# Kernel tuning notes

Measured on AMD Instinct MI355X. Metric: run time of the kernel, lower is better.

## Reference

```python
import jax, jax.numpy as jnp
import numpy as np

W = 10        # hurst window == signature path window (increments)
DELTA_MAX = 1.5
BN_EPS = 1e-5


def _revcumsum(x, axis):
    return jnp.flip(jnp.cumsum(jnp.flip(x, axis), axis=axis), axis)


def _forward(features, hw1, hb1, hw2, hb2, hw3, hb3, gw1, gb1, gw2, gb2,
             p1, p1b, p2, p2b, p3, p3b, p4, p4b,
             w1, b1, gamma, beta, rmean, rvar, w2, b2, w3, b3):
    B, T, d = features.shape
    f32 = features.dtype
    # log returns, left-padded with 0
    lp = features[:, :, 0]
    ret = jnp.pad(lp[:, 1:] - lp[:, :-1], ((0, 0), (1, 0)))
    # Hurst estimator on sliding windows returns[:, t-W:t] for t in [W, T)
    idxh = jnp.arange(T - W)[:, None] + jnp.arange(W)[None, :]
    rw = ret[:, idxh]                                          # [B, T-W, W]
    hh = jax.nn.relu(rw @ hw1 + hb1)
    hh = jax.nn.relu(hh @ hw2 + hb2)
    H_tail = 0.5 * jax.nn.sigmoid((hh @ hw3 + hb3)[..., 0])    # [B, T-W]
    # first W entries copy the t=W estimate (matches torch slice-broadcast)
    H_local = jnp.concatenate([jnp.repeat(H_tail[:, :1], W, axis=1), H_tail], axis=1)
    vol = jnp.cumsum(jnp.abs(ret), axis=1) / (jnp.arange(1, T + 1, dtype=f32) + 1e-8)
    # depth gate from (H_local, vol_local)
    regime = jnp.stack([H_local, vol], axis=-1)                # [B, T, 2]
    gate = jax.nn.softmax(jax.nn.relu(regime @ gw1 + gb1) @ gw2 + gb2, axis=-1)  # [B,T,4]
    # windowed path increments: window at t covers global increments t-W .. t-1
    Dinc = features[:, 1:] - features[:, :-1]                  # [B, T-1, d]
    Dp = jnp.pad(Dinc, ((0, 0), (W, 0), (0, 0)))
    idx = jnp.arange(T)[:, None] + jnp.arange(W)[None, :]
    Dw = Dp[:, idx]                                            # [B, T, W, d] (zero-padded early)
    S = _revcumsum(Dw, 2)                                      # suffix sums S_r = sum_{m>=r} D_m
    lvl1 = S[:, :, 0]                                          # [B, T, d] = path[-1]-path[0]
    # level2 (torch loop) = sum_{i<=m} D_i (x) D_m  (diagonal included)
    A = Dw[..., :, None] * S[..., None, :]                     # [B, T, W, d, d]
    l2f = jnp.sum(A, axis=2).reshape(B, T, d * d)
    # level3 (torch loop) = sum_{i<j<=n} D_i (x) D_j (x) D_n
    RA = _revcumsum(A, 2) - A                                  # exclusive suffix sum of A
    l3f = jnp.einsum('btrd,btref->btdef', Dw, RA).reshape(B, T, d ** 3)
    # level4 = flatten(level2 (x) level2); (d^2)^2 == d^4 so no pad/trunc
    l4f = (l2f[..., :, None] * l2f[..., None, :]).reshape(B, T, d ** 4)
    proj1 = lvl1 @ p1 + p1b
    proj2 = jnp.concatenate([lvl1, l2f], -1) @ p2 + p2b
    proj3 = jnp.concatenate([lvl1, l2f, l3f], -1) @ p3 + p3b
    proj4 = jnp.concatenate([lvl1, l2f, l3f, l4f], -1) @ p4 + p4b
    # depth k active iff path_len >= k+1 i.e. t >= k (k = depth index)
    tv = jnp.arange(T)
    m2 = (tv >= 1).astype(f32)[None, :, None]
    m3 = (tv >= 2).astype(f32)[None, :, None]
    m4 = (tv >= 3).astype(f32)[None, :, None]
    sig_repr = (gate[..., 0:1] * proj1 + m2 * gate[..., 1:2] * proj2
                + m3 * gate[..., 2:3] * proj3 + m4 * gate[..., 3:4] * proj4)
    combined = jnp.concatenate([sig_repr, features], axis=-1)  # [B, T, h+d]
    h1 = jax.nn.relu(combined @ w1 + b1)
    bn = gamma * (h1 - rmean) * jax.lax.rsqrt(rvar + BN_EPS) + beta  # BatchNorm1d (eval)
    h2 = jax.nn.relu(bn @ w2 + b2)
    return DELTA_MAX * jnp.tanh((h2 @ w3 + b3)[..., 0])        # [B, T]


def setup_inputs() -> dict:
    key = jax.random.key(0)
    ks = jax.random.split(key, 24)
    B, T, d, h = 32, 2048, 5, 64
    def w(k, shape, s=0.1):
        return (jax.random.normal(k, shape) * s).astype(jnp.float32)
    z = lambda n: jnp.zeros((n,), jnp.float32)
    return dict(
        features=0.1 * jax.random.normal(ks[0], (B, T, d), jnp.float32),
        hw1=w(ks[1], (10, 32)), hb1=z(32),
        hw2=w(ks[2], (32, 32)), hb2=z(32),
        hw3=w(ks[3], (32, 1)), hb3=z(1),
        gw1=w(ks[4], (2, 32)), gb1=z(32),
        gw2=w(ks[5], (32, 4)), gb2=z(4),
        p1=w(ks[6], (5, h)), p1b=z(h),
        p2=w(ks[7], (30, h)), p2b=z(h),
        p3=w(ks[8], (155, h)), p3b=z(h),
        p4=w(ks[9], (780, h)), p4b=z(h),
        w1=w(ks[10], (h + d, h)), b1=z(h),
        gamma=jnp.ones((h,), jnp.float32), beta=z(h),
        rmean=0.05 * jax.random.normal(ks[11], (h,), dtype=jnp.float32),
        rvar=jax.random.uniform(ks[12], (h,), jnp.float32, 0.5, 1.5),
        w2=w(ks[13], (h, h // 2)), b2=z(h // 2),
        w3=w(ks[14], (h // 2, 1)), b3=z(1),
    )


def reference(features, hw1, hb1, hw2, hb2, hw3, hb3, gw1, gb1, gw2, gb2,
              p1, p1b, p2, p2b, p3, p3b, p4, p4b,
              w1, b1, gamma, beta, rmean, rvar, w2, b2, w3, b3):
    return _forward(features, hw1, hb1, hw2, hb2, hw3, hb3, gw1, gb1, gw2, gb2,
                    p1, p1b, p2, p2b, p3, p3b, p4, p4b,
                    w1, b1, gamma, beta, rmean, rvar, w2, b2, w3, b3)
```

## Files before the change

### kernel.cpp

```cpp
#include <hip/hip_runtime.h>
#include <math.h>

#define TT 2048
#define W 10

typedef short bf16x8 __attribute__((ext_vector_type(8)));
typedef float f32x4 __attribute__((ext_vector_type(4)));

__device__ __forceinline__ unsigned short f32_bf16(float f) {
  unsigned int u = __float_as_uint(f);
  u = (u + 0x7fffu + ((u >> 16) & 1u)) >> 16;
  return (unsigned short)u;
}
__device__ __forceinline__ float bf16_f32(unsigned short h) {
  return __uint_as_float(((unsigned int)h) << 16);
}

__device__ __forceinline__ void wstore(unsigned short* WtH, unsigned short* WtL,
                                       int g, float v) {
  unsigned short hi = f32_bf16(v);
  WtH[g] = hi;
  WtL[g] = f32_bf16(v - bf16_f32(hi));
}

__global__ __launch_bounds__(256) void wprep_kernel(
    const float* __restrict__ p1, const float* __restrict__ p2,
    const float* __restrict__ p3, const float* __restrict__ p4,
    unsigned short* __restrict__ WtH, unsigned short* __restrict__ WtL) {
  int g = blockIdx.x * 256 + threadIdx.x;
  if (g < 2048) {
    int h = g / 32, k = g % 32;
    wstore(WtH, WtL, g, (k < 5) ? p1[k * 64 + h] : 0.f);
  } else if (g < 4096) {
    int loc = g - 2048, h = loc / 32, k = loc % 32;
    wstore(WtH, WtL, g, (k < 30) ? p2[k * 64 + h] : 0.f);
  } else if (g < 14336) {
    int loc = g - 4096, h = loc / 160, k = loc % 160;
    wstore(WtH, WtL, g, (k < 155) ? p3[k * 64 + h] : 0.f);
  } else {
    int loc = g - 14336, h = loc / 800, k = loc % 800;
    wstore(WtH, WtL, g, (k < 780) ? p4[k * 64 + h] : 0.f);
  }
}

__global__ __launch_bounds__(256) void prep_kernel(const float* __restrict__ F,
                                                   float* __restrict__ ret,
                                                   float* __restrict__ vol) {
  __shared__ float sAbs[TT];
  __shared__ float sPart[256];
  const int b = blockIdx.x, tid = threadIdx.x;
  const float* fb = F + (size_t)b * TT * 5;
#pragma unroll
  for (int u = 0; u < 8; ++u) {
    int t = u * 256 + tid;
    float rv = 0.f;
    if (t > 0) rv = fb[t * 5] - fb[(t - 1) * 5];
    ret[b * TT + t] = rv;
    sAbs[t] = fabsf(rv);
  }
  __syncthreads();
  float loc[8];
  float run = 0.f;
#pragma unroll
  for (int u = 0; u < 8; ++u) { run += sAbs[tid * 8 + u]; loc[u] = run; }
  sPart[tid] = run;
  __syncthreads();
  for (int off = 1; off < 256; off <<= 1) {
    float v = (tid >= off) ? sPart[tid - off] : 0.f;
    __syncthreads();
    sPart[tid] += v;
    __syncthreads();
  }
  float excl = sPart[tid] - run;
#pragma unroll
  for (int u = 0; u < 8; ++u) {
    int t = tid * 8 + u;
    vol[b * TT + t] = (excl + loc[u]) / ((float)(t + 1) + 1e-8f);
  }
}

__global__ __launch_bounds__(256) void gate_kernel(
    const float* __restrict__ ret, const float* __restrict__ vol,
    const float* __restrict__ hw1, const float* __restrict__ hb1,
    const float* __restrict__ hw2, const float* __restrict__ hb2,
    const float* __restrict__ hw3, const float* __restrict__ hb3,
    const float* __restrict__ gw1, const float* __restrict__ gb1,
    const float* __restrict__ gw2, const float* __restrict__ gb2,
    float* __restrict__ gate) {
  const int pos = blockIdx.x * 256 + threadIdx.x;
  const int t = pos & (TT - 1);
  const int start = (t >= W) ? (t - W) : 0;
  const float* rp = ret + (pos - t) + start;
  float r[W];
#pragma unroll
  for (int u = 0; u < W; ++u) r[u] = rp[u];
  float h1v[32];
#pragma unroll
  for (int j = 0; j < 32; ++j) {
    float a = hb1[j];
#pragma unroll
    for (int u = 0; u < W; ++u) a = fmaf(r[u], hw1[u * 32 + j], a);
    h1v[j] = fmaxf(a, 0.f);
  }
  float hs = hb3[0];
#pragma unroll
  for (int j = 0; j < 32; ++j) {
    float a = hb2[j];
#pragma unroll
    for (int u = 0; u < 32; ++u) a = fmaf(h1v[u], hw2[u * 32 + j], a);
    hs = fmaf(fmaxf(a, 0.f), hw3[j], hs);
  }
  const float H = 0.5f / (1.f + expf(-hs));
  const float vv = vol[pos];
  float l0 = gb2[0], l1 = gb2[1], l2 = gb2[2], l3 = gb2[3];
#pragma unroll
  for (int j = 0; j < 32; ++j) {
    float z = fmaxf(fmaf(H, gw1[j], fmaf(vv, gw1[32 + j], gb1[j])), 0.f);
    l0 = fmaf(z, gw2[j * 4 + 0], l0);
    l1 = fmaf(z, gw2[j * 4 + 1], l1);
    l2 = fmaf(z, gw2[j * 4 + 2], l2);
    l3 = fmaf(z, gw2[j * 4 + 3], l3);
  }
  float m = fmaxf(fmaxf(l0, l1), fmaxf(l2, l3));
  float e0 = expf(l0 - m), e1 = expf(l1 - m), e2 = expf(l2 - m), e3 = expf(l3 - m);
  float inv = 1.f / (e0 + e1 + e2 + e3);
  ((float4*)gate)[pos] = make_float4(e0 * inv, e1 * inv, e2 * inv, e3 * inv);
}

#define MFMA16(a, b, c) __builtin_amdgcn_mfma_f32_16x16x32_bf16((a), (b), (c), 0, 0, 0)

__global__ __launch_bounds__(256, 2) void sig_kernel(
    const float* __restrict__ F, const float* __restrict__ gate,
    const unsigned short* __restrict__ WtH, const unsigned short* __restrict__ WtL,
    const float* __restrict__ p1b, const float* __restrict__ p2b,
    const float* __restrict__ p3b, const float* __restrict__ p4b,
    const float* __restrict__ w1, const float* __restrict__ b1,
    const float* __restrict__ gam, const float* __restrict__ bet,
    const float* __restrict__ rmean, const float* __restrict__ rvar,
    const float* __restrict__ w2, const float* __restrict__ b2,
    const float* __restrict__ w3, const float* __restrict__ b3,
    float* __restrict__ out) {
  __shared__ unsigned short phiH[16][808];
  __shared__ unsigned short phiL[16][808];
  __shared__ float sUnion[2128];
  __shared__ float sFeat[80];

  float* sDw = sUnion;
  float* sS = sUnion + 800;
  float* sL2 = sUnion + 1600;

  const int tid = threadIdx.x;
  const int posBase = blockIdx.x * 16;

  for (int u = tid; u < 800; u += 256) {
    int p = u / 50, rr = u % 50;
    int r = rr / 5, i = rr % 5;
    int pos = posBase + p;
    int t = pos & (TT - 1);
    int q = t + r - W;
    float dv = 0.f;
    if (q >= 0) {
      const float* fb = F + (size_t)(pos - t) * 5;
      dv = fb[(q + 1) * 5 + i] - fb[q * 5 + i];
    }
    sDw[u] = dv;
  }
  for (int u = tid; u < 80; u += 256) sFeat[u] = F[(size_t)posBase * 5 + u];
  __syncthreads();

  for (int u = tid; u < 80; u += 256) {
    int p = u / 5, i = u % 5;
    float s = 0.f;
#pragma unroll
    for (int r = W - 1; r >= 0; --r) {
      s += sDw[p * 50 + r * 5 + i];
      sS[p * 50 + r * 5 + i] = s;
    }
    unsigned short hi = f32_bf16(s);
    phiH[p][i] = hi;
    phiL[p][i] = f32_bf16(s - bf16_f32(hi));
  }
  __syncthreads();

  for (int u = tid; u < 400; u += 256) {
    int p = u / 25, ef = u % 25;
    int e = ef / 5, fi = ef % 5;
    const float* dwp = sDw + p * 50;
    const float* sp = sS + p * 50;
    float a = 0.f;
    float l3a[5] = {0.f, 0.f, 0.f, 0.f, 0.f};
#pragma unroll
    for (int r = W - 1; r >= 0; --r) {
      float aa = a;
#pragma unroll
      for (int i = 0; i < 5; ++i) l3a[i] = fmaf(dwp[r * 5 + i], aa, l3a[i]);
      a = fmaf(dwp[r * 5 + e], sp[r * 5 + fi], a);
    }
    sL2[p * 25 + ef] = a;
    unsigned short hi = f32_bf16(a);
    phiH[p][5 + ef] = hi;
    phiL[p][5 + ef] = f32_bf16(a - bf16_f32(hi));
#pragma unroll
    for (int i = 0; i < 5; ++i) {
      int kk = 30 + i * 25 + ef;
      unsigned short h2i = f32_bf16(l3a[i]);
      phiH[p][kk] = h2i;
      phiL[p][kk] = f32_bf16(l3a[i] - bf16_f32(h2i));
    }
  }
  __syncthreads();

  for (int u = tid; u < 16 * 625; u += 256) {
    int p = u / 625, a2 = u % 625;
    float v = sL2[p * 25 + a2 / 25] * sL2[p * 25 + a2 % 25];
    int kk = 155 + a2;
    unsigned short hi = f32_bf16(v);
    phiH[p][kk] = hi;
    phiL[p][kk] = f32_bf16(v - bf16_f32(hi));
  }
  for (int u = tid; u < 16 * 28; u += 256) {
    int p = u / 28, kk = 780 + u % 28;
    phiH[p][kk] = 0;
    phiL[p][kk] = 0;
  }
  __syncthreads();

  const int lane = tid & 63, wv = tid >> 6;
  const int col = lane & 15, quad = lane >> 4;
  const int hw = wv * 16;

  const unsigned short* a4H = WtH + 14336 + (hw + col) * 800 + quad * 8;
  const unsigned short* a4L = WtL + 14336 + (hw + col) * 800 + quad * 8;
  const unsigned short* a3H = WtH + 4096 + (hw + col) * 160 + quad * 8;
  const unsigned short* a3L = WtL + 4096 + (hw + col) * 160 + quad * 8;
  const unsigned short* a2H = WtH + 2048 + (hw + col) * 32 + quad * 8;
  const unsigned short* a2L = WtL + 2048 + (hw + col) * 32 + quad * 8;
  const unsigned short* a1H = WtH + 0 + (hw + col) * 32 + quad * 8;
  const unsigned short* a1L = WtL + 0 + (hw + col) * 32 + quad * 8;
  const unsigned short* bH = &phiH[col][quad * 8];
  const unsigned short* bL = &phiL[col][quad * 8];

  f32x4 acc4a = {0.f, 0.f, 0.f, 0.f}, acc4b = {0.f, 0.f, 0.f, 0.f};
  f32x4 acc3a = {0.f, 0.f, 0.f, 0.f}, acc3b = {0.f, 0.f, 0.f, 0.f};
  f32x4 acc2 = {0.f, 0.f, 0.f, 0.f}, acc1 = {0.f, 0.f, 0.f, 0.f};

  for (int s = 0; s < 25; ++s) {
    bf16x8 bh = *(const bf16x8*)(bH + s * 32);
    bf16x8 bl = *(const bf16x8*)(bL + s * 32);
    bf16x8 ah = *(const bf16x8*)(a4H + s * 32);
    bf16x8 al = *(const bf16x8*)(a4L + s * 32);
    acc4a = MFMA16(ah, bh, acc4a);
    acc4b = MFMA16(ah, bl, acc4b);
    acc4b = MFMA16(al, bh, acc4b);
    if (s < 5) {
      bf16x8 ch = *(const bf16x8*)(a3H + s * 32);
      bf16x8 cl = *(const bf16x8*)(a3L + s * 32);
      acc3a = MFMA16(ch, bh, acc3a);
      acc3b = MFMA16(ch, bl, acc3b);
      acc3b = MFMA16(cl, bh, acc3b);
      if (s == 0) {
        bf16x8 dh = *(const bf16x8*)a2H;
        bf16x8 dl = *(const bf16x8*)a2L;
        acc2 = MFMA16(dh, bh, acc2);
        acc2 = MFMA16(dh, bl, acc2);
        acc2 = MFMA16(dl, bh, acc2);
        bf16x8 eh = *(const bf16x8*)a1H;
        bf16x8 el = *(const bf16x8*)a1L;
        acc1 = MFMA16(eh, bh, acc1);
        acc1 = MFMA16(eh, bl, acc1);
        acc1 = MFMA16(el, bh, acc1);
      }
    }
  }

  float* sSig = sUnion;
  float* sBn = sUnion + 1088;
  {
    f32x4 a4 = acc4a + acc4b;
    f32x4 a3 = acc3a + acc3b;
    const int pl = col;
    const int pos = posBase + pl;
    const int t = pos & (TT - 1);
    float4 g = ((const float4*)gate)[pos];
    float g0 = g.x;
    float g1 = (t >= 1) ? g.y : 0.f;
    float g2 = (t >= 2) ? g.z : 0.f;
    float g3 = (t >= 3) ? g.w : 0.f;
#pragma unroll
    for (int r = 0; r < 4; ++r) {
      int h = hw + quad * 4 + r;
      float v = g0 * (acc1[r] + p1b[h]) + g1 * (acc2[r] + p2b[h]) +
                g2 * (a3[r] + p3b[h]) + g3 * (a4[r] + p4b[h]);
      sSig[pl * 68 + h] = v;
    }
  }
  __syncthreads();

  {
    const int j = lane;
    float a0 = b1[j];
    float a1 = a0, a2 = a0, a3 = a0;
    const float* sg0 = sSig + (wv * 4 + 0) * 68;
    const float* sg1 = sSig + (wv * 4 + 1) * 68;
    const float* sg2 = sSig + (wv * 4 + 2) * 68;
    const float* sg3 = sSig + (wv * 4 + 3) * 68;
    for (int i = 0; i < 64; ++i) {
      float wt = w1[i * 64 + j];
      a0 = fmaf(sg0[i], wt, a0);
      a1 = fmaf(sg1[i], wt, a1);
      a2 = fmaf(sg2[i], wt, a2);
      a3 = fmaf(sg3[i], wt, a3);
    }
    const float* ft = sFeat + wv * 4 * 5;
#pragma unroll
    for (int i = 0; i < 5; ++i) {
      float wt = w1[(64 + i) * 64 + j];
      a0 = fmaf(ft[i], wt, a0);
      a1 = fmaf(ft[5 + i], wt, a1);
      a2 = fmaf(ft[10 + i], wt, a2);
      a3 = fmaf(ft[15 + i], wt, a3);
    }
    float sc = gam[j] * rsqrtf(rvar[j] + 1e-5f);
    float rm = rmean[j], be = bet[j];
    sBn[(wv * 4 + 0) * 65 + j] = fmaf(fmaxf(a0, 0.f) - rm, sc, be);
    sBn[(wv * 4 + 1) * 65 + j] = fmaf(fmaxf(a1, 0.f) - rm, sc, be);
    sBn[(wv * 4 + 2) * 65 + j] = fmaf(fmaxf(a2, 0.f) - rm, sc, be);
    sBn[(wv * 4 + 3) * 65 + j] = fmaf(fmaxf(a3, 0.f) - rm, sc, be);
  }
  __syncthreads();

  const float b3s = b3[0];
  for (int task = tid; task < 512; task += 256) {
    int p = task >> 5, k = task & 31;
    const float* bnp = sBn + p * 65;
    float a = b2[k];
    for (int j = 0; j < 64; ++j) a = fmaf(bnp[j], w2[j * 32 + k], a);
    float partial = fmaxf(a, 0.f) * w3[k];
#pragma unroll
    for (int off = 16; off >= 1; off >>= 1) partial += __shfl_xor(partial, off, 32);
    if (k == 0) out[posBase + p] = 1.5f * tanhf(partial + b3s);
  }
}

extern "C" void kernel_launch(void* const* d_in, const int* in_sizes, int n_in,
                              void* d_out, int out_size, void* d_ws, size_t ws_size,
                              hipStream_t stream) {
  const float* F = (const float*)d_in[0];
  const float* hw1 = (const float*)d_in[1];
  const float* hb1 = (const float*)d_in[2];
  const float* hw2 = (const float*)d_in[3];
  const float* hb2 = (const float*)d_in[4];
  const float* hw3 = (const float*)d_in[5];
  const float* hb3 = (const float*)d_in[6];
  const float* gw1 = (const float*)d_in[7];
  const float* gb1 = (const float*)d_in[8];
  const float* gw2 = (const float*)d_in[9];
  const float* gb2 = (const float*)d_in[10];
  const float* p1 = (const float*)d_in[11];
  const float* p1b = (const float*)d_in[12];
  const float* p2 = (const float*)d_in[13];
  const float* p2b = (const float*)d_in[14];
  const float* p3 = (const float*)d_in[15];
  const float* p3b = (const float*)d_in[16];
  const float* p4 = (const float*)d_in[17];
  const float* p4b = (const float*)d_in[18];
  const float* w1 = (const float*)d_in[19];
  const float* b1 = (const float*)d_in[20];
  const float* gam = (const float*)d_in[21];
  const float* bet = (const float*)d_in[22];
  const float* rmean = (const float*)d_in[23];
  const float* rvar = (const float*)d_in[24];
  const float* w2 = (const float*)d_in[25];
  const float* b2 = (const float*)d_in[26];
  const float* w3 = (const float*)d_in[27];
  const float* b3 = (const float*)d_in[28];

  float* ws = (float*)d_ws;
  float* ret = ws;
  float* vol = ws + 65536;
  float* gate = ws + 131072;
  unsigned short* WtH = (unsigned short*)(ws + 393216);
  unsigned short* WtL = WtH + 65536;
  float* out = (float*)d_out;

  wprep_kernel<<<256, 256, 0, stream>>>(p1, p2, p3, p4, WtH, WtL);
  prep_kernel<<<32, 256, 0, stream>>>(F, ret, vol);
  gate_kernel<<<256, 256, 0, stream>>>(ret, vol, hw1, hb1, hw2, hb2, hw3, hb3,
                                       gw1, gb1, gw2, gb2, gate);
  sig_kernel<<<4096, 256, 0, stream>>>(F, gate, WtH, WtL, p1b, p2b, p3b, p4b,
                                       w1, b1, gam, bet, rmean, rvar, w2, b2,
                                       w3, b3, out);
}
```

Baseline: 265.8 us.

## Factor level-4 signature projection, fuse gate MLP and weight prep into fewer kernels

The level-4 signature features (outer products of level-2 terms) are no longer materialized as 625 values per position. Their projection is instead computed as a sum of per-row MFMA products scaled by level-2 entries, with the p4 weights reshaped to match. The Hurst/gate MLP moves into the signature kernel, and weight prep merges into the prep kernel, cutting launches from four to two. Blocks now cover 32 positions with 512 threads, and bf16 hi/lo splitting switches from round-to-nearest to truncation, which slightly changes the numerics.

Measured after the change: 388.2 us. 46.1% more time.

```diff
diff --git a/kernel.cpp b/kernel.cpp
--- a/kernel.cpp
+++ b/kernel.cpp
@@ -7,62 +7,66 @@
 typedef short bf16x8 __attribute__((ext_vector_type(8)));
 typedef float f32x4 __attribute__((ext_vector_type(4)));
 
-__device__ __forceinline__ unsigned short f32_bf16(float f) {
-  unsigned int u = __float_as_uint(f);
-  u = (u + 0x7fffu + ((u >> 16) & 1u)) >> 16;
-  return (unsigned short)u;
+#define MFMA16(a, b, c) __builtin_amdgcn_mfma_f32_16x16x32_bf16((a), (b), (c), 0, 0, 0)
+
+__device__ __forceinline__ void splitTrunc(float v, unsigned short& hi,
+                                           unsigned short& lo) {
+  unsigned int u = __float_as_uint(v);
+  hi = (unsigned short)(u >> 16);
+  float r = v - __uint_as_float(u & 0xffff0000u);
+  lo = (unsigned short)(__float_as_uint(r) >> 16);
 }
-__device__ __forceinline__ float bf16_f32(unsigned short h) {
-  return __uint_as_float(((unsigned int)h) << 16);
-}
-
-__device__ __forceinline__ void wstore(unsigned short* WtH, unsigned short* WtL,
-                                       int g, float v) {
-  unsigned short hi = f32_bf16(v);
-  WtH[g] = hi;
-  WtL[g] = f32_bf16(v - bf16_f32(hi));
-}
-
-__global__ __launch_bounds__(256) void wprep_kernel(
-    const float* __restrict__ p1, const float* __restrict__ p2,
-    const float* __restrict__ p3, const float* __restrict__ p4,
-    unsigned short* __restrict__ WtH, unsigned short* __restrict__ WtL) {
-  int g = blockIdx.x * 256 + threadIdx.x;
-  if (g < 2048) {
-    int h = g / 32, k = g % 32;
-    wstore(WtH, WtL, g, (k < 5) ? p1[k * 64 + h] : 0.f);
-  } else if (g < 4096) {
-    int loc = g - 2048, h = loc / 32, k = loc % 32;
-    wstore(WtH, WtL, g, (k < 30) ? p2[k * 64 + h] : 0.f);
-  } else if (g < 14336) {
-    int loc = g - 4096, h = loc / 160, k = loc % 160;
-    wstore(WtH, WtL, g, (k < 155) ? p3[k * 64 + h] : 0.f);
-  } else {
-    int loc = g - 14336, h = loc / 800, k = loc % 800;
-    wstore(WtH, WtL, g, (k < 780) ? p4[k * 64 + h] : 0.f);
-  }
-}
-
-__global__ __launch_bounds__(256) void prep_kernel(const float* __restrict__ F,
-                                                   float* __restrict__ ret,
-                                                   float* __restrict__ vol) {
+
+__global__ __launch_bounds__(256) void prep_kernel(
+    const float* __restrict__ F, const float* __restrict__ p1,
+    const float* __restrict__ p2, const float* __restrict__ p3,
+    const float* __restrict__ p4, unsigned short* __restrict__ WtH,
+    unsigned short* __restrict__ WtL, float* __restrict__ ret,
+    float* __restrict__ vol) {
+  const int bid = blockIdx.x, tid = threadIdx.x;
+  if (bid >= 32) {
+    int g = (bid - 32) * 256 + tid;
+    float v;
+    if (g < 2048) {
+      int h = g >> 5, k = g & 31;
+      v = (k < 5) ? p1[k * 64 + h] : 0.f;
+    } else if (g < 4096) {
+      int loc = g - 2048, h = loc >> 5, k = loc & 31;
+      v = (k < 30) ? p2[k * 64 + h] : 0.f;
+    } else if (g < 14336) {
+      int loc = g - 4096, h = loc / 160, k = loc - h * 160;
+      v = (k < 155) ? p3[k * 64 + h] : 0.f;
+    } else if (g < 24576) {
+      int loc = g - 14336, h = loc / 160, k = loc - h * 160;
+      v = (k < 155) ? p4[k * 64 + h] : 0.f;
+    } else {
+      int loc = g - 24576, row = loc >> 5, j = loc & 31;
+      int i = row >> 6, h = row & 63;
+      v = (j < 25) ? p4[(155 + i * 25 + j) * 64 + h] : 0.f;
+    }
+    unsigned short hi, lo;
+    splitTrunc(v, hi, lo);
+    WtH[g] = hi;
+    WtL[g] = lo;
+    return;
+  }
   __shared__ float sAbs[TT];
   __shared__ float sPart[256];
-  const int b = blockIdx.x, tid = threadIdx.x;
-  const float* fb = F + (size_t)b * TT * 5;
+  const float* fb = F + (size_t)bid * TT * 5;
 #pragma unroll
   for (int u = 0; u < 8; ++u) {
     int t = u * 256 + tid;
-    float rv = 0.f;
-    if (t > 0) rv = fb[t * 5] - fb[(t - 1) * 5];
-    ret[b * TT + t] = rv;
+    float rv = (t > 0) ? (fb[t * 5] - fb[(t - 1) * 5]) : 0.f;
+    ret[bid * TT + t] = rv;
     sAbs[t] = fabsf(rv);
   }
   __syncthreads();
-  float loc[8];
-  float run = 0.f;
-#pragma unroll
-  for (int u = 0; u < 8; ++u) { run += sAbs[tid * 8 + u]; loc[u] = run; }
+  float loc8[8], run = 0.f;
+#pragma unroll
+  for (int u = 0; u < 8; ++u) {
+    run += sAbs[tid * 8 + u];
+    loc8[u] = run;
+  }
   sPart[tid] = run;
   __syncthreads();
   for (int off = 1; off < 256; off <<= 1) {
@@ -75,270 +79,332 @@
 #pragma unroll
   for (int u = 0; u < 8; ++u) {
     int t = tid * 8 + u;
-    vol[b * TT + t] = (excl + loc[u]) / ((float)(t + 1) + 1e-8f);
+    vol[bid * TT + t] = (excl + loc8[u]) / ((float)(t + 1) + 1e-8f);
   }
 }
 
-__global__ __launch_bounds__(256) void gate_kernel(
-    const float* __restrict__ ret, const float* __restrict__ vol,
-    const float* __restrict__ hw1, const float* __restrict__ hb1,
-    const float* __restrict__ hw2, const float* __restrict__ hb2,
-    const float* __restrict__ hw3, const float* __restrict__ hb3,
-    const float* __restrict__ gw1, const float* __restrict__ gb1,
-    const float* __restrict__ gw2, const float* __restrict__ gb2,
-    float* __restrict__ gate) {
-  const int pos = blockIdx.x * 256 + threadIdx.x;
-  const int t = pos & (TT - 1);
-  const int start = (t >= W) ? (t - W) : 0;
-  const float* rp = ret + (pos - t) + start;
-  float r[W];
-#pragma unroll
-  for (int u = 0; u < W; ++u) r[u] = rp[u];
-  float h1v[32];
-#pragma unroll
-  for (int j = 0; j < 32; ++j) {
-    float a = hb1[j];
-#pragma unroll
-    for (int u = 0; u < W; ++u) a = fmaf(r[u], hw1[u * 32 + j], a);
-    h1v[j] = fmaxf(a, 0.f);
-  }
-  float hs = hb3[0];
-#pragma unroll
-  for (int j = 0; j < 32; ++j) {
-    float a = hb2[j];
-#pragma unroll
-    for (int u = 0; u < 32; ++u) a = fmaf(h1v[u], hw2[u * 32 + j], a);
-    hs = fmaf(fmaxf(a, 0.f), hw3[j], hs);
-  }
-  const float H = 0.5f / (1.f + expf(-hs));
-  const float vv = vol[pos];
-  float l0 = gb2[0], l1 = gb2[1], l2 = gb2[2], l3 = gb2[3];
-#pragma unroll
-  for (int j = 0; j < 32; ++j) {
-    float z = fmaxf(fmaf(H, gw1[j], fmaf(vv, gw1[32 + j], gb1[j])), 0.f);
-    l0 = fmaf(z, gw2[j * 4 + 0], l0);
-    l1 = fmaf(z, gw2[j * 4 + 1], l1);
-    l2 = fmaf(z, gw2[j * 4 + 2], l2);
-    l3 = fmaf(z, gw2[j * 4 + 3], l3);
-  }
-  float m = fmaxf(fmaxf(l0, l1), fmaxf(l2, l3));
-  float e0 = expf(l0 - m), e1 = expf(l1 - m), e2 = expf(l2 - m), e3 = expf(l3 - m);
-  float inv = 1.f / (e0 + e1 + e2 + e3);
-  ((float4*)gate)[pos] = make_float4(e0 * inv, e1 * inv, e2 * inv, e3 * inv);
-}
-
-#define MFMA16(a, b, c) __builtin_amdgcn_mfma_f32_16x16x32_bf16((a), (b), (c), 0, 0, 0)
-
-__global__ __launch_bounds__(256, 2) void sig_kernel(
-    const float* __restrict__ F, const float* __restrict__ gate,
-    const unsigned short* __restrict__ WtH, const unsigned short* __restrict__ WtL,
-    const float* __restrict__ p1b, const float* __restrict__ p2b,
-    const float* __restrict__ p3b, const float* __restrict__ p4b,
-    const float* __restrict__ w1, const float* __restrict__ b1,
-    const float* __restrict__ gam, const float* __restrict__ bet,
-    const float* __restrict__ rmean, const float* __restrict__ rvar,
-    const float* __restrict__ w2, const float* __restrict__ b2,
-    const float* __restrict__ w3, const float* __restrict__ b3,
-    float* __restrict__ out) {
-  __shared__ unsigned short phiH[16][808];
-  __shared__ unsigned short phiL[16][808];
-  __shared__ float sUnion[2128];
-  __shared__ float sFeat[80];
-
-  float* sDw = sUnion;
-  float* sS = sUnion + 800;
-  float* sL2 = sUnion + 1600;
+__global__ __launch_bounds__(512, 6) void sig_kernel(
+    const float* __restrict__ F, const float* __restrict__ ret_g,
+    const float* __restrict__ vol_g, const unsigned short* __restrict__ WtH,
+    const unsigned short* __restrict__ WtL, const float* __restrict__ hw1,
+    const float* __restrict__ hb1, const float* __restrict__ hw2,
+    const float* __restrict__ hb2, const float* __restrict__ hw3,
+    const float* __restrict__ hb3, const float* __restrict__ gw1,
+    const float* __restrict__ gb1, const float* __restrict__ gw2,
+    const float* __restrict__ gb2, const float* __restrict__ p1b,
+    const float* __restrict__ p2b, const float* __restrict__ p3b,
+    const float* __restrict__ p4b, const float* __restrict__ w1,
+    const float* __restrict__ b1, const float* __restrict__ gam,
+    const float* __restrict__ bet, const float* __restrict__ rmean,
+    const float* __restrict__ rvar, const float* __restrict__ w2,
+    const float* __restrict__ b2, const float* __restrict__ w3,
+    const float* __restrict__ b3, float* __restrict__ out) {
+  __shared__ unsigned short phiH[32][168];
+  __shared__ unsigned short phiL[32][168];
+  __shared__ unsigned short l2bH[32][40];
+  __shared__ unsigned short l2bL[32][40];
+  __shared__ float sL2[32 * 25];
+  __shared__ __align__(16) float sF[44 * 8];
+  __shared__ float retl[42];
+  __shared__ float voll[32];
+  __shared__ float sGate[32 * 4];
+  __shared__ __align__(16) float sU[4352];
 
   const int tid = threadIdx.x;
-  const int posBase = blockIdx.x * 16;
-
-  for (int u = tid; u < 800; u += 256) {
-    int p = u / 50, rr = u % 50;
-    int r = rr / 5, i = rr % 5;
-    int pos = posBase + p;
-    int t = pos & (TT - 1);
-    int q = t + r - W;
-    float dv = 0.f;
-    if (q >= 0) {
-      const float* fb = F + (size_t)(pos - t) * 5;
-      dv = fb[(q + 1) * 5 + i] - fb[q * 5 + i];
-    }
-    sDw[u] = dv;
-  }
-  for (int u = tid; u < 80; u += 256) sFeat[u] = F[(size_t)posBase * 5 + u];
-  __syncthreads();
-
-  for (int u = tid; u < 80; u += 256) {
-    int p = u / 5, i = u % 5;
-    float s = 0.f;
-#pragma unroll
-    for (int r = W - 1; r >= 0; --r) {
-      s += sDw[p * 50 + r * 5 + i];
-      sS[p * 50 + r * 5 + i] = s;
-    }
-    unsigned short hi = f32_bf16(s);
-    phiH[p][i] = hi;
-    phiL[p][i] = f32_bf16(s - bf16_f32(hi));
-  }
-  __syncthreads();
-
-  for (int u = tid; u < 400; u += 256) {
-    int p = u / 25, ef = u % 25;
-    int e = ef / 5, fi = ef % 5;
-    const float* dwp = sDw + p * 50;
-    const float* sp = sS + p * 50;
-    float a = 0.f;
-    float l3a[5] = {0.f, 0.f, 0.f, 0.f, 0.f};
-#pragma unroll
-    for (int r = W - 1; r >= 0; --r) {
-      float aa = a;
-#pragma unroll
-      for (int i = 0; i < 5; ++i) l3a[i] = fmaf(dwp[r * 5 + i], aa, l3a[i]);
-      a = fmaf(dwp[r * 5 + e], sp[r * 5 + fi], a);
-    }
-    sL2[p * 25 + ef] = a;
-    unsigned short hi = f32_bf16(a);
-    phiH[p][5 + ef] = hi;
-    phiL[p][5 + ef] = f32_bf16(a - bf16_f32(hi));
-#pragma unroll
-    for (int i = 0; i < 5; ++i) {
-      int kk = 30 + i * 25 + ef;
-      unsigned short h2i = f32_bf16(l3a[i]);
-      phiH[p][kk] = h2i;
-      phiL[p][kk] = f32_bf16(l3a[i] - bf16_f32(h2i));
-    }
-  }
-  __syncthreads();
-
-  for (int u = tid; u < 16 * 625; u += 256) {
-    int p = u / 625, a2 = u % 625;
-    float v = sL2[p * 25 + a2 / 25] * sL2[p * 25 + a2 % 25];
-    int kk = 155 + a2;
-    unsigned short hi = f32_bf16(v);
-    phiH[p][kk] = hi;
-    phiL[p][kk] = f32_bf16(v - bf16_f32(hi));
-  }
-  for (int u = tid; u < 16 * 28; u += 256) {
-    int p = u / 28, kk = 780 + u % 28;
-    phiH[p][kk] = 0;
-    phiL[p][kk] = 0;
-  }
-  __syncthreads();
-
-  const int lane = tid & 63, wv = tid >> 6;
-  const int col = lane & 15, quad = lane >> 4;
-  const int hw = wv * 16;
-
-  const unsigned short* a4H = WtH + 14336 + (hw + col) * 800 + quad * 8;
-  const unsigned short* a4L = WtL + 14336 + (hw + col) * 800 + quad * 8;
-  const unsigned short* a3H = WtH + 4096 + (hw + col) * 160 + quad * 8;
-  const unsigned short* a3L = WtL + 4096 + (hw + col) * 160 + quad * 8;
-  const unsigned short* a2H = WtH + 2048 + (hw + col) * 32 + quad * 8;
-  const unsigned short* a2L = WtL + 2048 + (hw + col) * 32 + quad * 8;
-  const unsigned short* a1H = WtH + 0 + (hw + col) * 32 + quad * 8;
-  const unsigned short* a1L = WtL + 0 + (hw + col) * 32 + quad * 8;
-  const unsigned short* bH = &phiH[col][quad * 8];
-  const unsigned short* bL = &phiL[col][quad * 8];
-
-  f32x4 acc4a = {0.f, 0.f, 0.f, 0.f}, acc4b = {0.f, 0.f, 0.f, 0.f};
-  f32x4 acc3a = {0.f, 0.f, 0.f, 0.f}, acc3b = {0.f, 0.f, 0.f, 0.f};
-  f32x4 acc2 = {0.f, 0.f, 0.f, 0.f}, acc1 = {0.f, 0.f, 0.f, 0.f};
-
-  for (int s = 0; s < 25; ++s) {
-    bf16x8 bh = *(const bf16x8*)(bH + s * 32);
-    bf16x8 bl = *(const bf16x8*)(bL + s * 32);
-    bf16x8 ah = *(const bf16x8*)(a4H + s * 32);
-    bf16x8 al = *(const bf16x8*)(a4L + s * 32);
-    acc4a = MFMA16(ah, bh, acc4a);
-    acc4b = MFMA16(ah, bl, acc4b);
-    acc4b = MFMA16(al, bh, acc4b);
-    if (s < 5) {
-      bf16x8 ch = *(const bf16x8*)(a3H + s * 32);
-      bf16x8 cl = *(const bf16x8*)(a3L + s * 32);
+  const int b = blockIdx.x >> 6;
+  const int t0 = (blockIdx.x & 63) << 5;
+  const float* fb = F + (size_t)b * TT * 5;
+
+  for (int u = tid; u < 284; u += 512) {
+    if (u < 210) {
+      int j = u / 5, ch = u - 5 * j;
+      int t = t0 - 10 + j;
+      sF[j * 8 + ch] = (t >= 0) ? fb[t * 5 + ch] : 0.f;
+    } else if (u < 252) {
+      int jj = u - 210;
+      int t = t0 - 10 + jj;
+      retl[jj] = (t >= 0) ? ret_g[b * TT + t] : 0.f;
+    } else {
+      int p = u - 252;
+      voll[p] = vol_g[b * TT + t0 + p];
+    }
+  }
+  __syncthreads();
+
+  {
+    float* sH1 = sU;
+    const int p = tid >> 4, q = tid & 15;
+    const int t = t0 + p;
+    const int soff = (t >= W) ? p : (W - t0);
+    float r0[W];
+#pragma unroll
+    for (int u = 0; u < W; ++u) r0[u] = retl[soff + u];
+    const int j = q * 2;
+    float ax = hb1[j], ay = hb1[j + 1];
+#pragma unroll
+    for (int u = 0; u < W; ++u) {
+      float2 w = *(const float2*)&hw1[u * 32 + j];
+      ax = fmaf(r0[u], w.x, ax);
+      ay = fmaf(r0[u], w.y, ay);
+    }
+    sH1[p * 33 + j] = fmaxf(ax, 0.f);
+    sH1[p * 33 + j + 1] = fmaxf(ay, 0.f);
+    float bx = hb2[j], by = hb2[j + 1];
+    for (int u2 = 0; u2 < 32; ++u2) {
+      float hv = sH1[p * 33 + u2];
+      float2 w = *(const float2*)&hw2[u2 * 32 + j];
+      bx = fmaf(hv, w.x, bx);
+      by = fmaf(hv, w.y, by);
+    }
+    float hsp = fmaxf(bx, 0.f) * hw3[j] + fmaxf(by, 0.f) * hw3[j + 1];
+    hsp += __shfl_xor(hsp, 1);
+    hsp += __shfl_xor(hsp, 2);
+    hsp += __shfl_xor(hsp, 4);
+    hsp += __shfl_xor(hsp, 8);
+    float H = 0.5f / (1.f + expf(-(hsp + hb3[0])));
+    float vv = voll[p];
+    float l0 = 0.f, l1 = 0.f, l2v = 0.f, l3v = 0.f;
+#pragma unroll
+    for (int d = 0; d < 2; ++d) {
+      int j3 = q * 2 + d;
+      float z = fmaxf(fmaf(H, gw1[j3], fmaf(vv, gw1[32 + j3], gb1[j3])), 0.f);
+      l0 = fmaf(z, gw2[j3 * 4 + 0], l0);
+      l1 = fmaf(z, gw2[j3 * 4 + 1], l1);
+      l2v = fmaf(z, gw2[j3 * 4 + 2], l2v);
+      l3v = fmaf(z, gw2[j3 * 4 + 3], l3v);
+    }
+#pragma unroll
+    for (int m = 1; m <= 8; m <<= 1) {
+      l0 += __shfl_xor(l0, m);
+      l1 += __shfl_xor(l1, m);
+      l2v += __shfl_xor(l2v, m);
+      l3v += __shfl_xor(l3v, m);
+    }
+    if (q == 0) {
+      l0 += gb2[0]; l1 += gb2[1]; l2v += gb2[2]; l3v += gb2[3];
+      float mx = fmaxf(fmaxf(l0, l1), fmaxf(l2v, l3v));
+      float e0 = expf(l0 - mx), e1 = expf(l1 - mx);
+      float e2 = expf(l2v - mx), e3 = expf(l3v - mx);
+      float inv = 1.f / (e0 + e1 + e2 + e3);
+      *(float4*)&sGate[p * 4] = make_float4(e0 * inv, e1 * inv, e2 * inv, e3 * inv);
+    }
+  }
+
+  if (tid < 160) {
+    const int p = tid / 5, e = tid - 5 * (tid / 5);
+    float aA[5] = {0.f, 0.f, 0.f, 0.f, 0.f};
+    float sv[5] = {0.f, 0.f, 0.f, 0.f, 0.f};
+    float l3m[5][5];
+#pragma unroll
+    for (int i = 0; i < 5; ++i)
+#pragma unroll
+      for (int fi = 0; fi < 5; ++fi) l3m[i][fi] = 0.f;
+    float4 c4 = *(const float4*)&sF[(p + 10) * 8];
+    float ce = sF[(p + 10) * 8 + 4];
+    float cur[5] = {c4.x, c4.y, c4.z, c4.w, ce};
+#pragma unroll
+    for (int r = 9; r >= 0; --r) {
+      float4 n4 = *(const float4*)&sF[(p + r) * 8];
+      float ne = sF[(p + r) * 8 + 4];
+      float nxt[5] = {n4.x, n4.y, n4.z, n4.w, ne};
+      float m = ((t0 != 0) || (p + r >= 10)) ? 1.f : 0.f;
+      float d[5];
+#pragma unroll
+      for (int i = 0; i < 5; ++i) d[i] = (cur[i] - nxt[i]) * m;
+#pragma unroll
+      for (int fi = 0; fi < 5; ++fi) sv[fi] += d[fi];
+#pragma unroll
+      for (int i = 0; i < 5; ++i)
+#pragma unroll
+        for (int fi = 0; fi < 5; ++fi) l3m[i][fi] = fmaf(d[i], aA[fi], l3m[i][fi]);
+      float de = (e == 0) ? d[0] : (e == 1) ? d[1] : (e == 2) ? d[2]
+                : (e == 3) ? d[3] : d[4];
+#pragma unroll
+      for (int fi = 0; fi < 5; ++fi) aA[fi] = fmaf(de, sv[fi], aA[fi]);
+#pragma unroll
+      for (int i = 0; i < 5; ++i) cur[i] = nxt[i];
+    }
+    unsigned short hi, lo;
+#pragma unroll
+    for (int fi = 0; fi < 5; ++fi) {
+      float a = aA[fi];
+      int ef = e * 5 + fi;
+      sL2[p * 25 + ef] = a;
+      splitTrunc(a, hi, lo);
+      phiH[p][5 + ef] = hi;
+      phiL[p][5 + ef] = lo;
+      l2bH[p][ef] = hi;
+      l2bL[p][ef] = lo;
+#pragma unroll
+      for (int i = 0; i < 5; ++i) {
+        splitTrunc(l3m[i][fi], hi, lo);
+        phiH[p][30 + i * 25 + ef] = hi;
+        phiL[p][30 + i * 25 + ef] = lo;
+      }
+    }
+    if (e == 0) {
+#pragma unroll
+      for (int i = 0; i < 5; ++i) {
+        splitTrunc(sv[i], hi, lo);
+        phiH[p][i] = hi;
+        phiL[p][i] = lo;
+      }
+    }
+  } else {
+    for (int u = tid - 160; u < 384; u += 352) {
+      if (u < 160) {
+        int p = u / 5, k = 155 + (u - 5 * (u / 5));
+        phiH[p][k] = 0;
+        phiL[p][k] = 0;
+      } else {
+        int v = u - 160;
+        int p = v / 7, k = 25 + (v - 7 * (v / 7));
+        l2bH[p][k] = 0;
+        l2bL[p][k] = 0;
+      }
+    }
+  }
+  __syncthreads();
+
+  {
+    const int lane = tid & 63, wv = tid >> 6;
+    const int ptile = wv & 1, htile = wv >> 1;
+    const int col = lane & 15, quad = lane >> 4;
+    const int pl = ptile * 16 + col;
+    const int arow = htile * 16 + col;
+    const f32x4 z4 = {0.f, 0.f, 0.f, 0.f};
+    f32x4 acc1 = z4, acc2 = z4, acc3a = z4, acc3b = z4;
+    f32x4 acc4a = z4, acc4b = z4, acc4c = z4;
+
+    const unsigned short* W4aH = WtH + 14336 + arow * 160 + quad * 8;
+    const unsigned short* W4aL = WtL + 14336 + arow * 160 + quad * 8;
+    const unsigned short* W3H_ = WtH + 4096 + arow * 160 + quad * 8;
+    const unsigned short* W3L_ = WtL + 4096 + arow * 160 + quad * 8;
+#pragma unroll
+    for (int s = 0; s < 5; ++s) {
+      bf16x8 bh = *(const bf16x8*)&phiH[pl][s * 32 + quad * 8];
+      bf16x8 bl = *(const bf16x8*)&phiL[pl][s * 32 + quad * 8];
+      bf16x8 ah = *(const bf16x8*)(W4aH + s * 32);
+      bf16x8 al = *(const bf16x8*)(W4aL + s * 32);
+      acc4a = MFMA16(ah, bh, acc4a);
+      acc4b = MFMA16(ah, bl, acc4b);
+      acc4b = MFMA16(al, bh, acc4b);
+      bf16x8 ch = *(const bf16x8*)(W3H_ + s * 32);
+      bf16x8 cl = *(const bf16x8*)(W3L_ + s * 32);
       acc3a = MFMA16(ch, bh, acc3a);
       acc3b = MFMA16(ch, bl, acc3b);
       acc3b = MFMA16(cl, bh, acc3b);
       if (s == 0) {
-        bf16x8 dh = *(const bf16x8*)a2H;
-        bf16x8 dl = *(const bf16x8*)a2L;
+        bf16x8 dh = *(const bf16x8*)(WtH + 2048 + arow * 32 + quad * 8);
+        bf16x8 dl = *(const bf16x8*)(WtL + 2048 + arow * 32 + quad * 8);
         acc2 = MFMA16(dh, bh, acc2);
         acc2 = MFMA16(dh, bl, acc2);
         acc2 = MFMA16(dl, bh, acc2);
-        bf16x8 eh = *(const bf16x8*)a1H;
-        bf16x8 el = *(const bf16x8*)a1L;
+        bf16x8 eh = *(const bf16x8*)(WtH + arow * 32 + quad * 8);
+        bf16x8 el = *(const bf16x8*)(WtL + arow * 32 + quad * 8);
         acc1 = MFMA16(eh, bh, acc1);
         acc1 = MFMA16(eh, bl, acc1);
         acc1 = MFMA16(el, bh, acc1);
       }
     }
-  }
-
-  float* sSig = sUnion;
-  float* sBn = sUnion + 1088;
+    bf16x8 b2h = *(const bf16x8*)&l2bH[pl][quad * 8];
+    bf16x8 b2l = *(const bf16x8*)&l2bL[pl][quad * 8];
+    const unsigned short* W4bH = WtH + 24576 + arow * 32 + quad * 8;
+    const unsigned short* W4bL = WtL + 24576 + arow * 32 + quad * 8;
+    const float* l2row = sL2 + pl * 25;
+    for (int i = 0; i < 25; ++i) {
+      bf16x8 ah = *(const bf16x8*)(W4bH + i * 2048);
+      bf16x8 al = *(const bf16x8*)(W4bL + i * 2048);
+      f32x4 t4 = MFMA16(ah, b2h, z4);
+      t4 = MFMA16(ah, b2l, t4);
+      t4 = MFMA16(al, b2h, t4);
+      float scl = l2row[i];
+      acc4c[0] = fmaf(scl, t4[0], acc4c[0]);
+      acc4c[1] = fmaf(scl, t4[1], acc4c[1]);
+      acc4c[2] = fmaf(scl, t4[2], acc4c[2]);
+      acc4c[3] = fmaf(scl, t4[3], acc4c[3]);
+    }
+    const int t = t0 + pl;
+    float g0 = sGate[pl * 4 + 0];
+    float g1 = (t >= 1) ? sGate[pl * 4 + 1] : 0.f;
+    float g2 = (t >= 2) ? sGate[pl * 4 + 2] : 0.f;
+    float g3 = (t >= 3) ? sGate[pl * 4 + 3] : 0.f;
+    float* sSig = sU;
+#pragma unroll
+    for (int r = 0; r < 4; ++r) {
+      int h = htile * 16 + quad * 4 + r;
+      float v = g0 * (acc1[r] + p1b[h]) + g1 * (acc2[r] + p2b[h]) +
+                g2 * (acc3a[r] + acc3b[r] + p3b[h]) +
+                g3 * (acc4a[r] + acc4b[r] + acc4c[r] + p4b[h]);
+      sSig[pl * 68 + h] = v;
+    }
+  }
+  __syncthreads();
+
   {
-    f32x4 a4 = acc4a + acc4b;
-    f32x4 a3 = acc3a + acc3b;
-    const int pl = col;
-    const int pos = posBase + pl;
-    const int t = pos & (TT - 1);
-    float4 g = ((const float4*)gate)[pos];
-    float g0 = g.x;
-    float g1 = (t >= 1) ? g.y : 0.f;
-    float g2 = (t >= 2) ? g.z : 0.f;
-    float g3 = (t >= 3) ? g.w : 0.f;
-#pragma unroll
-    for (int r = 0; r < 4; ++r) {
-      int h = hw + quad * 4 + r;
-      float v = g0 * (acc1[r] + p1b[h]) + g1 * (acc2[r] + p2b[h]) +
-                g2 * (a3[r] + p3b[h]) + g3 * (a4[r] + p4b[h]);
-      sSig[pl * 68 + h] = v;
-    }
-  }
-  __syncthreads();
-
-  {
+    const float* sSig = sU;
+    float* sBn = sU + 2176;
+    const int lane = tid & 63, wv = tid >> 6;
     const int j = lane;
-    float a0 = b1[j];
-    float a1 = a0, a2 = a0, a3 = a0;
-    const float* sg0 = sSig + (wv * 4 + 0) * 68;
-    const float* sg1 = sSig + (wv * 4 + 1) * 68;
-    const float* sg2 = sSig + (wv * 4 + 2) * 68;
-    const float* sg3 = sSig + (wv * 4 + 3) * 68;
-    for (int i = 0; i < 64; ++i) {
-      float wt = w1[i * 64 + j];
-      a0 = fmaf(sg0[i], wt, a0);
-      a1 = fmaf(sg1[i], wt, a1);
-      a2 = fmaf(sg2[i], wt, a2);
-      a3 = fmaf(sg3[i], wt, a3);
-    }
-    const float* ft = sFeat + wv * 4 * 5;
+    const int p0 = wv * 4;
+    float a0 = b1[j], a1 = a0, a2 = a0, a3 = a0;
+    for (int i = 0; i < 64; i += 4) {
+      float4 s0 = *(const float4*)&sSig[(p0 + 0) * 68 + i];
+      float4 s1 = *(const float4*)&sSig[(p0 + 1) * 68 + i];
+      float4 s2 = *(const float4*)&sSig[(p0 + 2) * 68 + i];
+      float4 s3 = *(const float4*)&sSig[(p0 + 3) * 68 + i];
+      float wa = w1[(i + 0) * 64 + j];
+      float wb = w1[(i + 1) * 64 + j];
+      float wc = w1[(i + 2) * 64 + j];
+      float wd = w1[(i + 3) * 64 + j];
+      a0 = fmaf(s0.x, wa, a0); a0 = fmaf(s0.y, wb, a0);
+      a0 = fmaf(s0.z, wc, a0); a0 = fmaf(s0.w, wd, a0);
+      a1 = fmaf(s1.x, wa, a1); a1 = fmaf(s1.y, wb, a1);
+      a1 = fmaf(s1.z, wc, a1); a1 = fmaf(s1.w, wd, a1);
+      a2 = fmaf(s2.x, wa, a2); a2 = fmaf(s2.y, wb, a2);
+      a2 = fmaf(s2.z, wc, a2); a2 = fmaf(s2.w, wd, a2);
+      a3 = fmaf(s3.x, wa, a3); a3 = fmaf(s3.y, wb, a3);
+      a3 = fmaf(s3.z, wc, a3); a3 = fmaf(s3.w, wd, a3);
+    }
 #pragma unroll
     for (int i = 0; i < 5; ++i) {
       float wt = w1[(64 + i) * 64 + j];
-      a0 = fmaf(ft[i], wt, a0);
-      a1 = fmaf(ft[5 + i], wt, a1);
-      a2 = fmaf(ft[10 + i], wt, a2);
-      a3 = fmaf(ft[15 + i], wt, a3);
+      a0 = fmaf(sF[(p0 + 10) * 8 + i], wt, a0);
+      a1 = fmaf(sF[(p0 + 11) * 8 + i], wt, a1);
+      a2 = fmaf(sF[(p0 + 12) * 8 + i], wt, a2);
+      a3 = fmaf(sF[(p0 + 13) * 8 + i], wt, a3);
     }
     float sc = gam[j] * rsqrtf(rvar[j] + 1e-5f);
     float rm = rmean[j], be = bet[j];
-    sBn[(wv * 4 + 0) * 65 + j] = fmaf(fmaxf(a0, 0.f) - rm, sc, be);
-    sBn[(wv * 4 + 1) * 65 + j] = fmaf(fmaxf(a1, 0.f) - rm, sc, be);
-    sBn[(wv * 4 + 2) * 65 + j] = fmaf(fmaxf(a2, 0.f) - rm, sc, be);
-    sBn[(wv * 4 + 3) * 65 + j] = fmaf(fmaxf(a3, 0.f) - rm, sc, be);
-  }
-  __syncthreads();
-
-  const float b3s = b3[0];
-  for (int task = tid; task < 512; task += 256) {
-    int p = task >> 5, k = task & 31;
-    const float* bnp = sBn + p * 65;
-    float a = b2[k];
-    for (int j = 0; j < 64; ++j) a = fmaf(bnp[j], w2[j * 32 + k], a);
-    float partial = fmaxf(a, 0.f) * w3[k];
-#pragma unroll
-    for (int off = 16; off >= 1; off >>= 1) partial += __shfl_xor(partial, off, 32);
-    if (k == 0) out[posBase + p] = 1.5f * tanhf(partial + b3s);
+    sBn[(p0 + 0) * 68 + j] = fmaf(fmaxf(a0, 0.f) - rm, sc, be);
+    sBn[(p0 + 1) * 68 + j] = fmaf(fmaxf(a1, 0.f) - rm, sc, be);
+    sBn[(p0 + 2) * 68 + j] = fmaf(fmaxf(a2, 0.f) - rm, sc, be);
+    sBn[(p0 + 3) * 68 + j] = fmaf(fmaxf(a3, 0.f) - rm, sc, be);
+  }
+  __syncthreads();
+
+  {
+    const float* sBn = sU + 2176;
+    const float b3s = b3[0];
+#pragma unroll
+    for (int pass = 0; pass < 2; ++pass) {
+      int task = tid + pass * 512;
+      int p = task >> 5, k = task & 31;
+      const float* bnp = sBn + p * 68;
+      float a = b2[k];
+      for (int jj = 0; jj < 64; jj += 4) {
+        float4 bn4 = *(const float4*)&bnp[jj];
+        a = fmaf(bn4.x, w2[(jj + 0) * 32 + k], a);
+        a = fmaf(bn4.y, w2[(jj + 1) * 32 + k], a);
+        a = fmaf(bn4.z, w2[(jj + 2) * 32 + k], a);
+        a = fmaf(bn4.w, w2[(jj + 3) * 32 + k], a);
+      }
+      float partial = fmaxf(a, 0.f) * w3[k];
+#pragma unroll
+      for (int off = 16; off >= 1; off >>= 1)
+        partial += __shfl_xor(partial, off, 32);
+      if (k == 0) out[b * TT + t0 + p] = 1.5f * tanhf(partial + b3s);
+    }
   }
 }
 
@@ -378,16 +444,13 @@
   float* ws = (float*)d_ws;
   float* ret = ws;
   float* vol = ws + 65536;
-  float* gate = ws + 131072;
-  unsigned short* WtH = (unsigned short*)(ws + 393216);
-  unsigned short* WtL = WtH + 65536;
+  unsigned short* WtH = (unsigned short*)(ws + 131072);
+  unsigned short* WtL = WtH + 75776;
   float* out = (float*)d_out;
 
-  wprep_kernel<<<256, 256, 0, stream>>>(p1, p2, p3, p4, WtH, WtL);
-  prep_kernel<<<32, 256, 0, stream>>>(F, ret, vol);
-  gate_kernel<<<256, 256, 0, stream>>>(ret, vol, hw1, hb1, hw2, hb2, hw3, hb3,
-                                       gw1, gb1, gw2, gb2, gate);
-  sig_kernel<<<4096, 256, 0, stream>>>(F, gate, WtH, WtL, p1b, p2b, p3b, p4b,
-                                       w1, b1, gam, bet, rmean, rvar, w2, b2,
-                                       w3, b3, out);
+  prep_kernel<<<328, 256, 0, stream>>>(F, p1, p2, p3, p4, WtH, WtL, ret, vol);
+  sig_kernel<<<2048, 512, 0, stream>>>(F, ret, vol, WtH, WtL, hw1, hb1, hw2,
+                                       hb2, hw3, hb3, gw1, gb1, gw2, gb2, p1b,
+                                       p2b, p3b, p4b, w1, b1, gam, bet, rmean,
+                                       rvar, w2, b2, w3, b3, out);
 }
```
